# Kernel tuning notes

Hardware: AMD Instinct MI355X
Metric: run time of the kernel (lower is better)

The kernel has to match this reference:

```python
import jax, jax.numpy as jnp
import numpy as np

NEG = -1000000.0  # mask fill value used by the torch module


def setup_inputs() -> dict:
    key = jax.random.key(0)
    k1, k2, k3, k4 = jax.random.split(key, 4)
    B, L, D = 64, 1024, 64
    return {
        "queries": jax.random.normal(k1, (B, L, D), dtype=jnp.float32),
        "keys": jax.random.normal(k2, (B, L, D), dtype=jnp.float32),
        "values": jax.random.normal(k3, (B, L, D), dtype=jnp.float32),
        "valid_lens": jax.random.randint(k4, (B,), 1, 1024, dtype=jnp.int32),
    }


def reference(queries, keys, values, valid_lens):
    d = queries.shape[-1]
    # [B, Lq, Lk] attention scores
    scores = jnp.einsum("bqd,bkd->bqk", queries, keys) / jnp.sqrt(jnp.asarray(d, queries.dtype))
    Lk = scores.shape[-1]
    # sequence mask: key positions >= valid_len are filled with NEG (per batch)
    col = jnp.arange(Lk)  # [Lk]
    mask = col[None, None, :] >= valid_lens[:, None, None]  # [B, 1, Lk] -> broadcasts over q
    scores = jnp.where(mask, NEG, scores)
    attn = jax.nn.softmax(scores, axis=-1)
    # dropout p=0.0 (eval) -> identity
    return jnp.einsum("bqk,bkd->bqd", attn, values)
```

## Files before the change

### kernel.cpp

```cpp
#include <hip/hip_runtime.h>
#include <math.h>


typedef __attribute__((ext_vector_type(4))) float f32x4;
typedef __attribute__((ext_vector_type(8))) short bf16x8;
typedef __attribute__((ext_vector_type(8))) unsigned short u16x8;

constexpr int Bn = 64, Ln = 1024, Dn = 64;
constexpr float SCALE = 0.125f;

__device__ inline unsigned short f2bf(float x) {
    unsigned int u = __float_as_uint(x);
    return (unsigned short)((u + 0x7fffu + ((u >> 16) & 1u)) >> 16);
}

__global__ __launch_bounds__(256) void conv_bf16(const float* __restrict__ src,
                                                 unsigned short* __restrict__ dst, int n)
{
    int i = (blockIdx.x * 256 + threadIdx.x) * 8;
    if (i >= n) return;
    float4 a = *reinterpret_cast<const float4*>(src + i);
    float4 b = *reinterpret_cast<const float4*>(src + i + 4);
    u16x8 o;
    o[0] = f2bf(a.x); o[1] = f2bf(a.y); o[2] = f2bf(a.z); o[3] = f2bf(a.w);
    o[4] = f2bf(b.x); o[5] = f2bf(b.y); o[6] = f2bf(b.z); o[7] = f2bf(b.w);
    *reinterpret_cast<u16x8*>(dst + i) = o;
}

__global__ __launch_bounds__(256) void transp_v(const float* __restrict__ V,
                                                unsigned short* __restrict__ Vt)
{
    __shared__ float tile[64][65];
    const int b = blockIdx.x >> 4, kt = blockIdx.x & 15;
    const float* src = V + ((size_t)b * Ln + kt * 64) * Dn;
    const int tr = threadIdx.x >> 4;
    const int tc = threadIdx.x & 15;
    #pragma unroll
    for (int i = 0; i < 4; ++i) {
        int k = tr + i * 16;
        float4 v = *reinterpret_cast<const float4*>(src + (size_t)k * Dn + tc * 4);
        tile[k][tc * 4 + 0] = v.x; tile[k][tc * 4 + 1] = v.y;
        tile[k][tc * 4 + 2] = v.z; tile[k][tc * 4 + 3] = v.w;
    }
    __syncthreads();
    unsigned short* dst = Vt + (size_t)b * Dn * Ln + kt * 64;
    #pragma unroll
    for (int i = 0; i < 4; ++i) {
        int d = tr + i * 16;
        int k0 = tc * 4;
        ushort4 o;
        o.x = f2bf(tile[k0 + 0][d]); o.y = f2bf(tile[k0 + 1][d]);
        o.z = f2bf(tile[k0 + 2][d]); o.w = f2bf(tile[k0 + 3][d]);
        *reinterpret_cast<ushort4*>(dst + (size_t)d * Ln + k0) = o;
    }
}

__global__ __launch_bounds__(256) void flash_attn(
    const unsigned short* __restrict__ Qb,
    const unsigned short* __restrict__ Kb,
    const unsigned short* __restrict__ Vtb,
    const int* __restrict__ VL,
    float* __restrict__ O)
{
    __shared__ unsigned short kls[64 * 64];
    __shared__ unsigned short vls[64 * 64];
    __shared__ unsigned short plds[4][16 * 64];

    const int tid = threadIdx.x;
    const int w = tid >> 6, l = tid & 63;
    const int lg = l >> 4;
    const int ln = l & 15;
    const int b = blockIdx.x >> 4;
    const int qt = blockIdx.x & 15;
    const int qbase = qt * 64 + w * 16;
    const int valid = VL[b];
    const int nkt = (valid + 63) >> 6;

    const unsigned short* Qrow = Qb + ((size_t)b * Ln + qbase + ln) * Dn;
    const bf16x8 aq0 = *reinterpret_cast<const bf16x8*>(Qrow + lg * 8);
    const bf16x8 aq1 = *reinterpret_cast<const bf16x8*>(Qrow + 32 + lg * 8);

    f32x4 acc[4] = {{0.f,0.f,0.f,0.f},{0.f,0.f,0.f,0.f},{0.f,0.f,0.f,0.f},{0.f,0.f,0.f,0.f}};
    float mrow[4] = {-1e30f, -1e30f, -1e30f, -1e30f};
    float lrow[4] = {0.f, 0.f, 0.f, 0.f};

    const unsigned short* Kbase = Kb  + (size_t)b * Ln * Dn;
    const unsigned short* Vbase = Vtb + (size_t)b * Dn * Ln;
    unsigned short* pw = plds[w];

    for (int kt = 0; kt < nkt; ++kt) {
        __syncthreads();
        #pragma unroll
        for (int i = 0; i < 2; ++i) {
            int cid = tid + i * 256;
            int r = cid >> 3, c = cid & 7;
            int off = ((r * 128 + c * 16) ^ ((r & 7) << 4)) >> 1;
            u16x8 kv = *reinterpret_cast<const u16x8*>(Kbase + (size_t)(kt * 64 + r) * Dn + c * 8);
            *reinterpret_cast<u16x8*>(kls + off) = kv;
            u16x8 vv = *reinterpret_cast<const u16x8*>(Vbase + (size_t)r * Ln + kt * 64 + c * 8);
            *reinterpret_cast<u16x8*>(vls + off) = vv;
        }
        __syncthreads();

        f32x4 st[4] = {{0.f,0.f,0.f,0.f},{0.f,0.f,0.f,0.f},{0.f,0.f,0.f,0.f},{0.f,0.f,0.f,0.f}};
        #pragma unroll
        for (int t = 0; t < 4; ++t) {
            #pragma unroll
            for (int s = 0; s < 2; ++s) {
                int r = 16 * t + ln;
                int off = ((r * 128 + (lg * 8 + 32 * s) * 2) ^ ((r & 7) << 4)) >> 1;
                bf16x8 bk = *reinterpret_cast<const bf16x8*>(kls + off);
                st[t] = __builtin_amdgcn_mfma_f32_16x16x32_bf16(s == 0 ? aq0 : aq1, bk, st[t], 0, 0, 0);
            }
        }

        const int kbase = kt * 64;
        float sc[4][4];
        #pragma unroll
        for (int t = 0; t < 4; ++t) {
            bool msk = (kbase + 16 * t + ln) >= valid;
            #pragma unroll
            for (int j = 0; j < 4; ++j)
                sc[t][j] = msk ? -1e30f : st[t][j] * SCALE;
        }
        float mnew[4], rescale[4];
        #pragma unroll
        for (int j = 0; j < 4; ++j) {
            float mx = fmaxf(fmaxf(sc[0][j], sc[1][j]), fmaxf(sc[2][j], sc[3][j]));
            #pragma unroll
            for (int off = 8; off >= 1; off >>= 1) mx = fmaxf(mx, __shfl_xor(mx, off, 64));
            mnew[j] = fmaxf(mrow[j], mx);
            rescale[j] = __expf(mrow[j] - mnew[j]);
            mrow[j] = mnew[j];
        }
        #pragma unroll
        for (int j = 0; j < 4; ++j) {
            float rs = 0.f;
            const int q = lg * 4 + j;
            #pragma unroll
            for (int t = 0; t < 4; ++t) {
                float p = __expf(sc[t][j] - mnew[j]);
                rs += p;
                int col = 16 * t + ln;
                int off = ((q * 128 + col * 2) ^ ((q & 7) << 4)) >> 1;
                pw[off] = f2bf(p);
            }
            #pragma unroll
            for (int off = 8; off >= 1; off >>= 1) rs += __shfl_xor(rs, off, 64);
            lrow[j] = lrow[j] * rescale[j] + rs;
            #pragma unroll
            for (int t = 0; t < 4; ++t) acc[t][j] *= rescale[j];
        }
        __syncthreads();

        #pragma unroll
        for (int s = 0; s < 2; ++s) {
            int poff = ((ln * 128 + (lg * 8 + 32 * s) * 2) ^ ((ln & 7) << 4)) >> 1;
            bf16x8 pa = *reinterpret_cast<const bf16x8*>(pw + poff);
            #pragma unroll
            for (int t = 0; t < 4; ++t) {
                int r = 16 * t + ln;
                int voff = ((r * 128 + (lg * 8 + 32 * s) * 2) ^ ((r & 7) << 4)) >> 1;
                bf16x8 bv = *reinterpret_cast<const bf16x8*>(vls + voff);
                acc[t] = __builtin_amdgcn_mfma_f32_16x16x32_bf16(pa, bv, acc[t], 0, 0, 0);
            }
        }
    }

    float inv[4];
    #pragma unroll
    for (int j = 0; j < 4; ++j) inv[j] = 1.0f / lrow[j];
    float* Orow = O + ((size_t)b * Ln + qbase) * Dn;
    #pragma unroll
    for (int t = 0; t < 4; ++t) {
        #pragma unroll
        for (int j = 0; j < 4; ++j) {
            int q = lg * 4 + j;
            int d = 16 * t + ln;
            Orow[(size_t)q * Dn + d] = acc[t][j] * inv[j];
        }
    }
}

extern "C" void kernel_launch(void* const* d_in, const int* in_sizes, int n_in,
                              void* d_out, int out_size, void* d_ws, size_t ws_size,
                              hipStream_t stream) {
    const float* Q = (const float*)d_in[0];
    const float* K = (const float*)d_in[1];
    const float* V = (const float*)d_in[2];
    const int* VL = (const int*)d_in[3];
    float* O = (float*)d_out;

    const int n = Bn * Ln * Dn;
    unsigned short* Qb  = (unsigned short*)d_ws;
    unsigned short* Kbb = Qb + (size_t)n;
    unsigned short* Vtb = Kbb + (size_t)n;

    conv_bf16<<<n / 8 / 256, 256, 0, stream>>>(Q, Qb, n);
    conv_bf16<<<n / 8 / 256, 256, 0, stream>>>(K, Kbb, n);
    transp_v<<<Bn * 16, 256, 0, stream>>>(V, Vtb);
    flash_attn<<<Bn * 16, 256, 0, stream>>>(Qb, Kbb, Vtb, VL, O);
}
```

Measured before the change: 145.7 us.

## Fuse bf16 conversion and V transpose into flash attention with prefetch and lazy rescale

Drops the separate conversion and V-transpose kernels and reads fp32 Q/K/V directly in the attention kernel, converting to bf16 while filling shared memory. The next K/V tile is prefetched into registers while the current one is computed. The softmax scale and log2(e) are folded into Q so exp2f can be used, masking runs only on the boundary tile, and the online-softmax rescale is skipped unless the running max grows by more than a threshold. The kernel also removes the barrier between P writes and P reads, relying on each warp touching only its own P buffer. The cost is doing fp32 loads and conversions redundantly across the 16 query tiles per batch, plus higher register pressure from the prefetch.

Measured after the change: 137.7 us. -5.5%, faster.

```diff
diff --git a/kernel.cpp b/kernel.cpp
--- a/kernel.cpp
+++ b/kernel.cpp
@@ -7,59 +7,17 @@
 typedef __attribute__((ext_vector_type(8))) unsigned short u16x8;
 
 constexpr int Bn = 64, Ln = 1024, Dn = 64;
-constexpr float SCALE = 0.125f;
+constexpr float QSCALE = 0.125f * 1.44269504088896340736f;
+constexpr float DEFER_THR = 10.0f;
 
 __device__ inline unsigned short f2bf(float x) {
     unsigned int u = __float_as_uint(x);
     return (unsigned short)((u + 0x7fffu + ((u >> 16) & 1u)) >> 16);
 }
 
-__global__ __launch_bounds__(256) void conv_bf16(const float* __restrict__ src,
-                                                 unsigned short* __restrict__ dst, int n)
-{
-    int i = (blockIdx.x * 256 + threadIdx.x) * 8;
-    if (i >= n) return;
-    float4 a = *reinterpret_cast<const float4*>(src + i);
-    float4 b = *reinterpret_cast<const float4*>(src + i + 4);
-    u16x8 o;
-    o[0] = f2bf(a.x); o[1] = f2bf(a.y); o[2] = f2bf(a.z); o[3] = f2bf(a.w);
-    o[4] = f2bf(b.x); o[5] = f2bf(b.y); o[6] = f2bf(b.z); o[7] = f2bf(b.w);
-    *reinterpret_cast<u16x8*>(dst + i) = o;
-}
-
-__global__ __launch_bounds__(256) void transp_v(const float* __restrict__ V,
-                                                unsigned short* __restrict__ Vt)
-{
-    __shared__ float tile[64][65];
-    const int b = blockIdx.x >> 4, kt = blockIdx.x & 15;
-    const float* src = V + ((size_t)b * Ln + kt * 64) * Dn;
-    const int tr = threadIdx.x >> 4;
-    const int tc = threadIdx.x & 15;
-    #pragma unroll
-    for (int i = 0; i < 4; ++i) {
-        int k = tr + i * 16;
-        float4 v = *reinterpret_cast<const float4*>(src + (size_t)k * Dn + tc * 4);
-        tile[k][tc * 4 + 0] = v.x; tile[k][tc * 4 + 1] = v.y;
-        tile[k][tc * 4 + 2] = v.z; tile[k][tc * 4 + 3] = v.w;
-    }
-    __syncthreads();
-    unsigned short* dst = Vt + (size_t)b * Dn * Ln + kt * 64;
-    #pragma unroll
-    for (int i = 0; i < 4; ++i) {
-        int d = tr + i * 16;
-        int k0 = tc * 4;
-        ushort4 o;
-        o.x = f2bf(tile[k0 + 0][d]); o.y = f2bf(tile[k0 + 1][d]);
-        o.z = f2bf(tile[k0 + 2][d]); o.w = f2bf(tile[k0 + 3][d]);
-        *reinterpret_cast<ushort4*>(dst + (size_t)d * Ln + k0) = o;
-    }
-}
-
 __global__ __launch_bounds__(256) void flash_attn(
-    const unsigned short* __restrict__ Qb,
-    const unsigned short* __restrict__ Kb,
-    const unsigned short* __restrict__ Vtb,
-    const int* __restrict__ VL,
+    const float* __restrict__ Q, const float* __restrict__ K,
+    const float* __restrict__ V, const int* __restrict__ VL,
     float* __restrict__ O)
 {
     __shared__ unsigned short kls[64 * 64];
@@ -68,100 +26,146 @@
 
     const int tid = threadIdx.x;
     const int w = tid >> 6, l = tid & 63;
-    const int lg = l >> 4;
-    const int ln = l & 15;
+    const int lg = l >> 4, ln = l & 15;
     const int b = blockIdx.x >> 4;
     const int qt = blockIdx.x & 15;
     const int qbase = qt * 64 + w * 16;
     const int valid = VL[b];
     const int nkt = (valid + 63) >> 6;
 
-    const unsigned short* Qrow = Qb + ((size_t)b * Ln + qbase + ln) * Dn;
-    const bf16x8 aq0 = *reinterpret_cast<const bf16x8*>(Qrow + lg * 8);
-    const bf16x8 aq1 = *reinterpret_cast<const bf16x8*>(Qrow + 32 + lg * 8);
+    const float* Kbase = K + (size_t)b * Ln * Dn;
+    const float* Vbase = V + (size_t)b * Ln * Dn;
+
+    bf16x8 aq0, aq1;
+    {
+        const f32x4* qp = reinterpret_cast<const f32x4*>(Q + ((size_t)b * Ln + qbase + ln) * Dn);
+        f32x4 q0 = qp[lg * 2], q1 = qp[lg * 2 + 1], q2 = qp[8 + lg * 2], q3 = qp[8 + lg * 2 + 1];
+        #pragma unroll
+        for (int j = 0; j < 4; ++j) {
+            aq0[j]     = (short)f2bf(q0[j] * QSCALE);
+            aq0[j + 4] = (short)f2bf(q1[j] * QSCALE);
+            aq1[j]     = (short)f2bf(q2[j] * QSCALE);
+            aq1[j + 4] = (short)f2bf(q3[j] * QSCALE);
+        }
+    }
+
+    const int kr = tid >> 2, kc = (tid & 3) * 16;
+    const int vd = l, vk0 = w * 16;
+
+    f32x4 kpre[4];
+    float vpre[16];
+    {
+        const f32x4* kp = reinterpret_cast<const f32x4*>(Kbase + (size_t)kr * Dn + kc);
+        #pragma unroll
+        for (int i = 0; i < 4; ++i) kpre[i] = kp[i];
+        const float* vp = Vbase + (size_t)vk0 * Dn + vd;
+        #pragma unroll
+        for (int i = 0; i < 16; ++i) vpre[i] = vp[(size_t)i * Dn];
+    }
 
     f32x4 acc[4] = {{0.f,0.f,0.f,0.f},{0.f,0.f,0.f,0.f},{0.f,0.f,0.f,0.f},{0.f,0.f,0.f,0.f}};
     float mrow[4] = {-1e30f, -1e30f, -1e30f, -1e30f};
     float lrow[4] = {0.f, 0.f, 0.f, 0.f};
-
-    const unsigned short* Kbase = Kb  + (size_t)b * Ln * Dn;
-    const unsigned short* Vbase = Vtb + (size_t)b * Dn * Ln;
     unsigned short* pw = plds[w];
+    char* klsb = reinterpret_cast<char*>(kls);
+    char* vlsb = reinterpret_cast<char*>(vls);
+    char* pwb  = reinterpret_cast<char*>(pw);
 
     for (int kt = 0; kt < nkt; ++kt) {
         __syncthreads();
-        #pragma unroll
-        for (int i = 0; i < 2; ++i) {
-            int cid = tid + i * 256;
-            int r = cid >> 3, c = cid & 7;
-            int off = ((r * 128 + c * 16) ^ ((r & 7) << 4)) >> 1;
-            u16x8 kv = *reinterpret_cast<const u16x8*>(Kbase + (size_t)(kt * 64 + r) * Dn + c * 8);
-            *reinterpret_cast<u16x8*>(kls + off) = kv;
-            u16x8 vv = *reinterpret_cast<const u16x8*>(Vbase + (size_t)r * Ln + kt * 64 + c * 8);
-            *reinterpret_cast<u16x8*>(vls + off) = vv;
+        {
+            u16x8 c0, c1;
+            #pragma unroll
+            for (int j = 0; j < 4; ++j) {
+                c0[j]     = f2bf(kpre[0][j]);  c0[j + 4] = f2bf(kpre[1][j]);
+                c1[j]     = f2bf(kpre[2][j]);  c1[j + 4] = f2bf(kpre[3][j]);
+            }
+            const int kb = kr * 128 + kc * 2, ksw = (kr & 7) << 4;
+            *reinterpret_cast<u16x8*>(klsb + ((kb)      ^ ksw)) = c0;
+            *reinterpret_cast<u16x8*>(klsb + ((kb + 16) ^ ksw)) = c1;
+            u16x8 v0, v1;
+            #pragma unroll
+            for (int j = 0; j < 8; ++j) { v0[j] = f2bf(vpre[j]); v1[j] = f2bf(vpre[j + 8]); }
+            const int vb = vd * 128 + vk0 * 2, vsw = (vd & 7) << 4;
+            *reinterpret_cast<u16x8*>(vlsb + ((vb)      ^ vsw)) = v0;
+            *reinterpret_cast<u16x8*>(vlsb + ((vb + 16) ^ vsw)) = v1;
         }
         __syncthreads();
+
+        if (kt + 1 < nkt) {
+            const f32x4* kp = reinterpret_cast<const f32x4*>(Kbase + (size_t)((kt + 1) * 64 + kr) * Dn + kc);
+            #pragma unroll
+            for (int i = 0; i < 4; ++i) kpre[i] = kp[i];
+            const float* vp = Vbase + (size_t)((kt + 1) * 64 + vk0) * Dn + vd;
+            #pragma unroll
+            for (int i = 0; i < 16; ++i) vpre[i] = vp[(size_t)i * Dn];
+        }
 
         f32x4 st[4] = {{0.f,0.f,0.f,0.f},{0.f,0.f,0.f,0.f},{0.f,0.f,0.f,0.f},{0.f,0.f,0.f,0.f}};
         #pragma unroll
         for (int t = 0; t < 4; ++t) {
+            const int r = 16 * t + ln, rsw = (r & 7) << 4;
+            bf16x8 bk0 = *reinterpret_cast<const bf16x8*>(klsb + ((r * 128 + lg * 16)      ^ rsw));
+            st[t] = __builtin_amdgcn_mfma_f32_16x16x32_bf16(aq0, bk0, st[t], 0, 0, 0);
+            bf16x8 bk1 = *reinterpret_cast<const bf16x8*>(klsb + ((r * 128 + lg * 16 + 64) ^ rsw));
+            st[t] = __builtin_amdgcn_mfma_f32_16x16x32_bf16(aq1, bk1, st[t], 0, 0, 0);
+        }
+
+        const int kbase = kt * 64;
+        if (kbase + 64 > valid) {
             #pragma unroll
-            for (int s = 0; s < 2; ++s) {
-                int r = 16 * t + ln;
-                int off = ((r * 128 + (lg * 8 + 32 * s) * 2) ^ ((r & 7) << 4)) >> 1;
-                bf16x8 bk = *reinterpret_cast<const bf16x8*>(kls + off);
-                st[t] = __builtin_amdgcn_mfma_f32_16x16x32_bf16(s == 0 ? aq0 : aq1, bk, st[t], 0, 0, 0);
+            for (int t = 0; t < 4; ++t) {
+                const bool msk = (kbase + 16 * t + ln) >= valid;
+                #pragma unroll
+                for (int j = 0; j < 4; ++j) if (msk) st[t][j] = -1e30f;
             }
         }
 
-        const int kbase = kt * 64;
-        float sc[4][4];
-        #pragma unroll
-        for (int t = 0; t < 4; ++t) {
-            bool msk = (kbase + 16 * t + ln) >= valid;
-            #pragma unroll
-            for (int j = 0; j < 4; ++j)
-                sc[t][j] = msk ? -1e30f : st[t][j] * SCALE;
-        }
-        float mnew[4], rescale[4];
+        float mx[4];
         #pragma unroll
         for (int j = 0; j < 4; ++j) {
-            float mx = fmaxf(fmaxf(sc[0][j], sc[1][j]), fmaxf(sc[2][j], sc[3][j]));
+            float m0 = fmaxf(fmaxf(st[0][j], st[1][j]), fmaxf(st[2][j], st[3][j]));
             #pragma unroll
-            for (int off = 8; off >= 1; off >>= 1) mx = fmaxf(mx, __shfl_xor(mx, off, 64));
-            mnew[j] = fmaxf(mrow[j], mx);
-            rescale[j] = __expf(mrow[j] - mnew[j]);
-            mrow[j] = mnew[j];
+            for (int off = 8; off >= 1; off >>= 1) m0 = fmaxf(m0, __shfl_xor(m0, off, 64));
+            mx[j] = m0;
+        }
+        const float g = fmaxf(fmaxf(mx[0] - mrow[0], mx[1] - mrow[1]),
+                              fmaxf(mx[2] - mrow[2], mx[3] - mrow[3]));
+        if (__any(g > DEFER_THR)) {
+            #pragma unroll
+            for (int j = 0; j < 4; ++j) {
+                const float mn = fmaxf(mrow[j], mx[j]);
+                const float rs = exp2f(mrow[j] - mn);
+                mrow[j] = mn;
+                lrow[j] *= rs;
+                #pragma unroll
+                for (int t = 0; t < 4; ++t) acc[t][j] *= rs;
+            }
         }
         #pragma unroll
         for (int j = 0; j < 4; ++j) {
+            const int q = lg * 4 + j, qsw = (q & 7) << 4;
             float rs = 0.f;
-            const int q = lg * 4 + j;
             #pragma unroll
             for (int t = 0; t < 4; ++t) {
-                float p = __expf(sc[t][j] - mnew[j]);
+                const float p = exp2f(st[t][j] - mrow[j]);
                 rs += p;
-                int col = 16 * t + ln;
-                int off = ((q * 128 + col * 2) ^ ((q & 7) << 4)) >> 1;
-                pw[off] = f2bf(p);
+                const int col = 16 * t + ln;
+                *reinterpret_cast<unsigned short*>(pwb + ((q * 128 + col * 2) ^ qsw)) = f2bf(p);
             }
             #pragma unroll
             for (int off = 8; off >= 1; off >>= 1) rs += __shfl_xor(rs, off, 64);
-            lrow[j] = lrow[j] * rescale[j] + rs;
-            #pragma unroll
-            for (int t = 0; t < 4; ++t) acc[t][j] *= rescale[j];
+            lrow[j] += rs;
         }
-        __syncthreads();
 
         #pragma unroll
         for (int s = 0; s < 2; ++s) {
-            int poff = ((ln * 128 + (lg * 8 + 32 * s) * 2) ^ ((ln & 7) << 4)) >> 1;
-            bf16x8 pa = *reinterpret_cast<const bf16x8*>(pw + poff);
+            bf16x8 pa = *reinterpret_cast<const bf16x8*>(
+                pwb + ((ln * 128 + lg * 16 + 64 * s) ^ ((ln & 7) << 4)));
             #pragma unroll
             for (int t = 0; t < 4; ++t) {
-                int r = 16 * t + ln;
-                int voff = ((r * 128 + (lg * 8 + 32 * s) * 2) ^ ((r & 7) << 4)) >> 1;
-                bf16x8 bv = *reinterpret_cast<const bf16x8*>(vls + voff);
+                const int r = 16 * t + ln, rsw = (r & 7) << 4;
+                bf16x8 bv = *reinterpret_cast<const bf16x8*>(vlsb + ((r * 128 + lg * 16 + 64 * s) ^ rsw));
                 acc[t] = __builtin_amdgcn_mfma_f32_16x16x32_bf16(pa, bv, acc[t], 0, 0, 0);
             }
         }
@@ -175,8 +179,8 @@
     for (int t = 0; t < 4; ++t) {
         #pragma unroll
         for (int j = 0; j < 4; ++j) {
-            int q = lg * 4 + j;
-            int d = 16 * t + ln;
+            const int q = lg * 4 + j;
+            const int d = 16 * t + ln;
             Orow[(size_t)q * Dn + d] = acc[t][j] * inv[j];
         }
     }
@@ -190,14 +194,5 @@
     const float* V = (const float*)d_in[2];
     const int* VL = (const int*)d_in[3];
     float* O = (float*)d_out;
-
-    const int n = Bn * Ln * Dn;
-    unsigned short* Qb  = (unsigned short*)d_ws;
-    unsigned short* Kbb = Qb + (size_t)n;
-    unsigned short* Vtb = Kbb + (size_t)n;
-
-    conv_bf16<<<n / 8 / 256, 256, 0, stream>>>(Q, Qb, n);
-    conv_bf16<<<n / 8 / 256, 256, 0, stream>>>(K, Kbb, n);
-    transp_v<<<Bn * 16, 256, 0, stream>>>(V, Vtb);
-    flash_attn<<<Bn * 16, 256, 0, stream>>>(Qb, Kbb, Vtb, VL, O);
+    flash_attn<<<Bn * 16, 256, 0, stream>>>(Q, K, V, VL, O);
 }
```
